# Kernel tuning notes

Measured on AMD Instinct MI355X. Metric: run time of the kernel, lower is better.

## Reference

```python
import jax, jax.numpy as jnp
import numpy as np

B, L, D = 128, 196, 512
T = 20
V, E, H, A = 10000, 256, 512, 512


def setup_inputs() -> dict:
    key = jax.random.key(0)
    ks = jax.random.split(key, 20)
    s = lambda *sh: 0.02
    inp = {
        "a": jax.random.normal(ks[0], (B, L, D), jnp.float32),
        "captions": jax.random.randint(ks[1], (B, T), 0, V),
        "lengths": jnp.full((B,), T, dtype=jnp.int64),
        "embed_W": jax.random.normal(ks[2], (V, E), jnp.float32) * 0.02,
        "Wa": jax.random.normal(ks[3], (D, A), jnp.float32) * 0.02,
        "Wh": jax.random.normal(ks[4], (H, A), jnp.float32) * 0.02,
        "Wc": jax.random.normal(ks[5], (H, A), jnp.float32) * 0.02,
        "v": jax.random.normal(ks[6], (A,), jnp.float32) * 0.02,
        "beta_W": jax.random.normal(ks[7], (H, 1), jnp.float32) * 0.02,
        "beta_b": jnp.zeros((1,), jnp.float32),
        "W_ih": jax.random.normal(ks[8], (E + D, 4 * H), jnp.float32) * 0.02,
        "W_hh": jax.random.normal(ks[9], (H, 4 * H), jnp.float32) * 0.02,
        "b_ih": jnp.zeros((4 * H,), jnp.float32),
        "b_hh": jnp.zeros((4 * H,), jnp.float32),
        "fc_W": jax.random.normal(ks[10], (H, V), jnp.float32) * 0.02,
        "fc_b": jnp.zeros((V,), jnp.float32),
        "initW_h": jax.random.normal(ks[11], (D, H), jnp.float32) * 0.02,
        "initb_h": jnp.zeros((H,), jnp.float32),
        "initW_c": jax.random.normal(ks[12], (D, H), jnp.float32) * 0.02,
        "initb_c": jnp.zeros((H,), jnp.float32),
    }
    return inp


def _decode(a, captions, embed_W, Wa, Wh, Wc, v, beta_W, beta_b,
            W_ih, W_hh, b_ih, b_hh, fc_W, fc_b,
            initW_h, initb_h, initW_c, initb_c):
    # dropout layers are treated as identity (eval mode) for a deterministic reference
    emb = embed_W[captions]                       # (B, T, E)
    mean_ctx = a.mean(axis=1)                     # (B, D)
    h0 = jnp.tanh(mean_ctx @ initW_h + initb_h)   # (B, H)
    c0 = jnp.tanh(mean_ctx @ initW_c + initb_c)
    wa = a @ Wa                                   # (B, L, A), hoisted (invariant over t)
    Hd = h0.shape[-1]

    def step(carry, x_t):
        h, c, prev_h = carry
        # dual additive attention: scores from annotations + h + prev_h (context_input)
        score = jnp.tanh(wa + (h @ Wh)[:, None, :] + (prev_h @ Wc)[:, None, :])  # (B,L,A)
        e = score @ v                                                            # (B,L)
        alpha = jax.nn.softmax(e, axis=1)
        beta = jax.nn.sigmoid(h @ beta_W + beta_b)                               # (B,1)
        ctx = beta * jnp.einsum('bl,bld->bd', alpha, a)                          # (B,D)
        # LSTMCell
        x = jnp.concatenate([x_t, ctx], axis=1)                                  # (B,E+D)
        gates = x @ W_ih + b_ih + h @ W_hh + b_hh                                # (B,4H)
        i, f, g, o = jnp.split(gates, 4, axis=1)
        c_new = jax.nn.sigmoid(f) * c + jax.nn.sigmoid(i) * jnp.tanh(g)
        h_new = jax.nn.sigmoid(o) * jnp.tanh(c_new)
        logits_t = h_new @ fc_W + fc_b                                           # (B,V)
        return (h_new, c_new, h_new), (logits_t, alpha)

    xs = jnp.swapaxes(emb[:, :T - 1, :], 0, 1)    # (T-1, B, E) time-major
    _, (logits_t, alphas_t) = jax.lax.scan(step, (h0, c0, h0), xs)
    # all lengths == T: pack_padded_sequence(batch_first=True).data is time-major flatten
    packed_logits = logits_t.reshape((T - 1) * a.shape[0], -1)                   # ((T-1)*B, V)
    alphas = jnp.swapaxes(alphas_t, 0, 1)                                        # (B, T-1, L)
    return packed_logits, alphas


def reference(a, captions, lengths, embed_W, Wa, Wh, Wc, v, beta_W, beta_b,
              W_ih, W_hh, b_ih, b_hh, fc_W, fc_b,
              initW_h, initb_h, initW_c, initb_c):
    return _decode(a, captions, embed_W, Wa, Wh, Wc, v, beta_W, beta_b,
                   W_ih, W_hh, b_ih, b_hh, fc_W, fc_b,
                   initW_h, initb_h, initW_c, initb_c)
```

## Files before the change

kernel.cpp:

```cpp
#include <hip/hip_runtime.h>
#include <hip/hip_bf16.h>
#include <math.h>

#define B_ 128
#define L_ 196
#define D_ 512
#define T_ 20
#define V_ 10000
#define E_ 256
#define H_ 512
#define A_ 512
#define TM1 19
#define ROWS (TM1*B_)
#define G4H 2048
#define KCAT 1024
#define LH 98

typedef unsigned short ushort_t;
typedef __attribute__((ext_vector_type(8))) short bf16x8;
typedef __attribute__((ext_vector_type(4))) float f32x4;

__device__ __forceinline__ float fast_tanh(float x){
    float ax = fabsf(x);
    float e = __expf(-2.f*ax);
    float r = __builtin_amdgcn_rcpf(1.f + e);
    return copysignf((1.f - e)*r, x);
}
__device__ __forceinline__ float sigmoidf_(float x){
    return __builtin_amdgcn_rcpf(1.f + __expf(-x));
}
__device__ __forceinline__ ushort_t f2b(float f){
    union{float f; unsigned u;} x; x.f = f;
    unsigned r = x.u + 0x7fffu + ((x.u>>16)&1u);
    return (ushort_t)(r>>16);
}
__device__ __forceinline__ float b2f(ushort_t h){
    union{unsigned u; float f;} x; x.u = ((unsigned)h)<<16;
    return x.f;
}
__device__ __forceinline__ float b2f_lo(unsigned u){ union{unsigned u; float f;} x; x.u = u<<16; return x.f; }
__device__ __forceinline__ float b2f_hi(unsigned u){ union{unsigned u; float f;} x; x.u = u & 0xffff0000u; return x.f; }

#define GL16(gsrc, ldst) __builtin_amdgcn_global_load_lds( \
    (const __attribute__((address_space(1))) unsigned*)(gsrc), \
    (__attribute__((address_space(3))) unsigned*)(ldst), 16, 0, 0)

__global__ __launch_bounds__(256)
void gemm_logits_k(const ushort_t* __restrict__ A, int lda,
                   const ushort_t* __restrict__ BT, int ldb,
                   float* __restrict__ C, int ldc,
                   int N, int K, const float* __restrict__ bias)
{
    __shared__ ushort_t As[2][4096];
    __shared__ ushort_t Bs[2][4096];
    int bid = blockIdx.x;
    int swz = (bid & 7)*190 + (bid >> 3);
    int mt = swz % 19, nt = swz / 19;
    if (nt >= 79) return;
    const int bm = mt*128, bn = nt*128;
    const int tid = threadIdx.x;
    const int lane = tid & 63;
    const int wave = tid >> 6;
    const int wm = (wave >> 1) * 64;
    const int wn = (wave & 1) * 64;
    const int lrow = lane & 15;
    const int lk8  = (lane >> 4) * 8;
    const int srow = tid >> 2;
    const int skq0 = (tid & 3) * 8;
    const int wbase = wave * 512;

    f32x4 acc[4][4];
    #pragma unroll
    for (int i=0;i<4;i++)
        #pragma unroll
        for (int j=0;j<4;j++) acc[i][j] = (f32x4){0.f,0.f,0.f,0.f};

    const ushort_t* Ab = A  + (size_t)(bm+srow)*lda + skq0;
    const ushort_t* Bb = BT + (size_t)(bn+srow)*ldb + skq0;

    GL16(Ab,                    &As[0][wbase]);
    GL16(Ab + (size_t)64*lda,   &As[0][2048 + wbase]);
    GL16(Bb,                    &Bs[0][wbase]);
    GL16(Bb + (size_t)64*ldb,   &Bs[0][2048 + wbase]);

    int buf = 0;
    for (int k0 = 0; k0 < K; k0 += 32) {
        asm volatile("s_waitcnt vmcnt(0)" ::: "memory");
        __syncthreads();
        if (k0 + 32 < K){
            int nb = buf ^ 1;
            GL16(Ab + k0 + 32,                  &As[nb][wbase]);
            GL16(Ab + (size_t)64*lda + k0 + 32, &As[nb][2048 + wbase]);
            GL16(Bb + k0 + 32,                  &Bs[nb][wbase]);
            GL16(Bb + (size_t)64*ldb + k0 + 32, &Bs[nb][2048 + wbase]);
        }
        bf16x8 af[4], bfr[4];
        #pragma unroll
        for (int i=0;i<4;i++) af[i]  = *(bf16x8*)&As[buf][(wm + i*16 + lrow)*32 + lk8];
        #pragma unroll
        for (int j=0;j<4;j++) bfr[j] = *(bf16x8*)&Bs[buf][(wn + j*16 + lrow)*32 + lk8];
        #pragma unroll
        for (int i=0;i<4;i++)
            #pragma unroll
            for (int j=0;j<4;j++)
                acc[i][j] = __builtin_amdgcn_mfma_f32_16x16x32_bf16(af[i], bfr[j], acc[i][j], 0, 0, 0);
        buf ^= 1;
    }

    const int rq = (lane >> 4) * 4;
    float* eps = (float*)As;
    #pragma unroll
    for (int c = 0; c < 4; ++c){
        __syncthreads();
        if ((wave >> 1) == (c >> 1)){
            const int ib = 2*(c & 1);
            #pragma unroll
            for (int ii = 0; ii < 2; ++ii){
                #pragma unroll
                for (int j = 0; j < 4; ++j){
                    #pragma unroll
                    for (int q = 0; q < 4; ++q){
                        int lr_ = ii*16 + rq + q;
                        int lc  = wn + j*16 + lrow;
                        eps[lr_*128 + lc] = acc[ib+ii][j][q];
                    }
                }
            }
        }
        __syncthreads();
        for (int it = tid; it < 1024; it += 256){
            int r = it >> 5, c4 = it & 31;
            int col0 = bn + c4*4;
            if (col0 >= N) continue;
            f32x4 vv = *(f32x4*)&eps[r*128 + c4*4];
            float* dst = &C[(size_t)(bm + 32*c + r)*ldc + col0];
            if (col0 + 3 < N){
                float4 bb = *(const float4*)(bias + col0);
                vv[0] += bb.x; vv[1] += bb.y; vv[2] += bb.z; vv[3] += bb.w;
                __builtin_nontemporal_store(vv, (f32x4*)dst);
            } else {
                for (int e=0; e<4 && col0+e < N; ++e)
                    __builtin_nontemporal_store(vv[e] + bias[col0+e], dst + e);
            }
        }
    }
}

struct GJob { const ushort_t* A; int lda; const ushort_t* BT; int ldb;
              void* C; int ldc; int N, K; const float* bias; int out_bf16; int nx; int nblk; };

__global__ __launch_bounds__(256) void gemm_dual_k(GJob j0, GJob j1){
    __shared__ ushort_t As[2][4096];
    __shared__ ushort_t Bs[2][4096];
    int bid = blockIdx.x;
    GJob jb = (bid < j0.nblk) ? j0 : j1;
    if (bid >= j0.nblk) bid -= j0.nblk;
    const int bn = (bid % jb.nx)*128, bm = (bid / jb.nx)*128;
    const int tid = threadIdx.x;
    const int lane = tid & 63;
    const int wave = tid >> 6;
    const int wm = (wave >> 1) * 64;
    const int wn = (wave & 1) * 64;
    const int lrow = lane & 15;
    const int lk8  = (lane >> 4) * 8;
    const int srow = tid >> 2;
    const int skq0 = (tid & 3) * 8;
    const int wbase = wave * 512;

    f32x4 acc[4][4];
    #pragma unroll
    for (int i=0;i<4;i++)
        #pragma unroll
        for (int j=0;j<4;j++) acc[i][j] = (f32x4){0.f,0.f,0.f,0.f};

    const ushort_t* Ab = jb.A  + (size_t)(bm+srow)*jb.lda + skq0;
    const ushort_t* Bb = jb.BT + (size_t)(bn+srow)*jb.ldb + skq0;

    GL16(Ab,                        &As[0][wbase]);
    GL16(Ab + (size_t)64*jb.lda,    &As[0][2048 + wbase]);
    GL16(Bb,                        &Bs[0][wbase]);
    GL16(Bb + (size_t)64*jb.ldb,    &Bs[0][2048 + wbase]);

    int buf = 0;
    for (int k0 = 0; k0 < jb.K; k0 += 32) {
        asm volatile("s_waitcnt vmcnt(0)" ::: "memory");
        __syncthreads();
        if (k0 + 32 < jb.K){
            int nb = buf ^ 1;
            GL16(Ab + k0 + 32,                      &As[nb][wbase]);
            GL16(Ab + (size_t)64*jb.lda + k0 + 32,  &As[nb][2048 + wbase]);
            GL16(Bb + k0 + 32,                      &Bs[nb][wbase]);
            GL16(Bb + (size_t)64*jb.ldb + k0 + 32,  &Bs[nb][2048 + wbase]);
        }
        bf16x8 af[4], bfr[4];
        #pragma unroll
        for (int i=0;i<4;i++) af[i]  = *(bf16x8*)&As[buf][(wm + i*16 + lrow)*32 + lk8];
        #pragma unroll
        for (int j=0;j<4;j++) bfr[j] = *(bf16x8*)&Bs[buf][(wn + j*16 + lrow)*32 + lk8];
        #pragma unroll
        for (int i=0;i<4;i++)
            #pragma unroll
            for (int j=0;j<4;j++)
                acc[i][j] = __builtin_amdgcn_mfma_f32_16x16x32_bf16(af[i], bfr[j], acc[i][j], 0, 0, 0);
        buf ^= 1;
    }

    const int rq = (lane >> 4) * 4;
    #pragma unroll
    for (int j=0;j<4;j++){
        int col = bn + wn + j*16 + lrow;
        if (col >= jb.N) continue;
        float bv = jb.bias ? jb.bias[col] : 0.f;
        #pragma unroll
        for (int i=0;i<4;i++){
            #pragma unroll
            for (int q=0;q<4;q++){
                int row = bm + wm + i*16 + rq + q;
                float v = acc[i][j][q] + bv;
                if (jb.out_bf16) ((ushort_t*)jb.C)[(size_t)row*jb.ldc + col] = f2b(v);
                else             ((float*)jb.C)[(size_t)row*jb.ldc + col] = v;
            }
        }
    }
}

__global__ __launch_bounds__(256) void gemm64t2(const float* __restrict__ Amcp, int lda,
                       const float* __restrict__ B0, const float* __restrict__ B1, int ldb,
                       float* __restrict__ C0, float* __restrict__ C1, int ldc,
                       const float* __restrict__ bias0, const float* __restrict__ bias1)
{
    const float* Bm  = blockIdx.z ? B1 : B0;
    float* C         = blockIdx.z ? C1 : C0;
    const float* bias= blockIdx.z ? bias1 : bias0;
    __shared__ float As[16][65];
    __shared__ float Bs[16][65];
    int bm = blockIdx.y*64, bn = blockIdx.x*64;
    int tid = threadIdx.x;
    int tx = tid & 15, ty = tid >> 4;
    const float invL = 1.f/(float)L_;
    float acc[4][4] = {};
    for (int k0 = 0; k0 < D_; k0 += 16) {
        {
            int r  = tid >> 2;
            int kq = (tid & 3) * 4;
            const float* Ap = Amcp + (size_t)(bm+r)*lda + k0 + kq;
            float4 v0 = *(const float4*)(Ap);
            float4 v1 = *(const float4*)(Ap + 65536);
            float4 v2 = *(const float4*)(Ap + 131072);
            float4 v3 = *(const float4*)(Ap + 196608);
            float4 va = make_float4((v0.x+v1.x+v2.x+v3.x)*invL, (v0.y+v1.y+v2.y+v3.y)*invL,
                                    (v0.z+v1.z+v2.z+v3.z)*invL, (v0.w+v1.w+v2.w+v3.w)*invL);
            As[kq+0][r]=va.x; As[kq+1][r]=va.y; As[kq+2][r]=va.z; As[kq+3][r]=va.w;
        }
        {
            int kk = tid >> 4;
            int nq = (tid & 15) * 4;
            float4 vb = *(const float4*)(Bm + (size_t)(k0+kk)*ldb + bn + nq);
            Bs[kk][nq+0]=vb.x; Bs[kk][nq+1]=vb.y; Bs[kk][nq+2]=vb.z; Bs[kk][nq+3]=vb.w;
        }
        __syncthreads();
        #pragma unroll
        for (int k = 0; k < 16; ++k) {
            float a0[4], b0[4];
            #pragma unroll
            for (int i=0;i<4;i++) a0[i] = As[k][ty*4+i];
            #pragma unroll
            for (int j=0;j<4;j++) b0[j] = Bs[k][tx*4+j];
            #pragma unroll
            for (int i=0;i<4;i++)
                #pragma unroll
                for (int j=0;j<4;j++)
                    acc[i][j] = fmaf(a0[i], b0[j], acc[i][j]);
        }
        __syncthreads();
    }
    #pragma unroll
    for (int i=0;i<4;i++){
        int row = bm + ty*4 + i;
        #pragma unroll
        for (int j=0;j<4;j++){
            int col = bn + tx*4 + j;
            C[(size_t)row*ldc + col] = fast_tanh(acc[i][j] + bias[col]);
        }
    }
}

struct TJob { const float* src; const float* src2; ushort_t* dst;
              int lds, Ksz, Nsz, koff, ldk, nx, nblk; };
struct PrepArgs {
    TJob j[6];
    const float* a; ushort_t* a_b; float* mcp;
    const float* b_ih; const float* b_hh; float* bias4h; unsigned* bars;
    const int* caps; const float* embW; ushort_t* xemb;
};

__global__ __launch_bounds__(256) void prep_all_k(PrepArgs P){
    __shared__ float t[32][33];
    int bid = blockIdx.x;
    const int tid = threadIdx.x;
    if (bid < 256){
        const int b = bid >> 1, half = bid & 1;
        const int quad = tid & 127;
        const int sl = tid >> 7;
        const int pi = half*2 + sl;
        const int l0 = half*LH + sl*49;
        const float* p = P.a + ((size_t)(b*L_ + l0))*D_ + quad*4;
        ushort_t* q = P.a_b + ((size_t)(b*L_ + l0))*D_ + quad*4;
        float4 s = make_float4(0.f,0.f,0.f,0.f);
        for (int l=0;l<49;l++){
            float4 v = *(const float4*)(p + (size_t)l*D_);
            s.x += v.x; s.y += v.y; s.z += v.z; s.w += v.w;
            ushort_t r[4] = {f2b(v.x),f2b(v.y),f2b(v.z),f2b(v.w)};
            *(uint2*)(q + (size_t)l*D_) = *(uint2*)r;
        }
        *(float4*)(P.mcp + (size_t)pi*65536 + (size_t)b*D_ + quad*4) = s;
        return;
    }
    bid -= 256;
    if (bid < 8128){
        int ji = 0;
        while (bid >= P.j[ji].nblk){ bid -= P.j[ji].nblk; ji++; }
        const TJob jb = P.j[ji];
        int n0 = (bid % jb.nx)*32, k0 = (bid / jb.nx)*32;
        int tx = tid & 31, ty = tid >> 5;
        #pragma unroll
        for (int kk = ty; kk < 32; kk += 8){
            int k = k0 + kk, n = n0 + tx;
            float v = 0.f;
            if (k < jb.Ksz && n < jb.Nsz){
                v = jb.src[(size_t)k*jb.lds + n];
                if (jb.src2) v += jb.src2[(size_t)k*jb.lds + n];
            }
            t[kk][tx] = v;
        }
        __syncthreads();
        #pragma unroll
        for (int nn = ty; nn < 32; nn += 8){
            int n = n0 + nn, k = k0 + tx;
            if (k < jb.Ksz) jb.dst[(size_t)n*jb.ldk + jb.koff + k] = f2b(t[tx][nn]);
        }
        return;
    }
    bid -= 8128;
    if (bid == 0){
        for (int k = tid; k < G4H; k += 256) P.bias4h[k] = P.b_ih[k] + P.b_hh[k];
        P.bars[tid] = 0u;
        return;
    }
    bid -= 1;
    int i = bid*4 + (tid >> 6);
    int lane = tid & 63;
    int tt = i / B_, b = i - tt*B_;
    int cap = P.caps[b*T_ + tt];
    float4 v = ((const float4*)(P.embW + (size_t)cap*E_))[lane];
    ushort_t r[4] = {f2b(v.x),f2b(v.y),f2b(v.z),f2b(v.w)};
    *(uint2*)(P.xemb + (size_t)i*E_ + lane*4) = *(uint2*)r;
}

__global__ __launch_bounds__(512) void hw0cvt_k(const float* __restrict__ h0f,
                        const ushort_t* __restrict__ WhcT, const float* __restrict__ beta_W,
                        ushort_t* __restrict__ xcat, float* __restrict__ hWp, float* __restrict__ bdot){
    int b = blockIdx.x, tid = threadIdx.x;
    int lane = tid & 63, wave = tid >> 6;
    __shared__ ushort_t hls[512];
    __shared__ float rr[8];
    float hv = h0f[b*H_ + tid];
    ushort_t hb = f2b(hv);
    xcat[(size_t)b*KCAT + D_ + tid] = hb;
    hls[tid] = hb;
    hWp[(size_t)(b*2+1)*512 + tid] = 0.f;
    float dv = hv * beta_W[tid];
    #pragma unroll
    for (int off=32; off; off>>=1) dv += __shfl_down(dv, off);
    if (lane==0) rr[wave] = dv;
    __syncthreads();
    if (tid == 0){
        float s = rr[0]+rr[1]+rr[2]+rr[3]+rr[4]+rr[5]+rr[6]+rr[7];
        bdot[b*2] = s; bdot[b*2+1] = 0.f;
    }
    int wn = wave * 64;
    int col16 = lane & 15;
    int khi = (lane >> 4) * 8;
    bool a_on = (col16 == 0);
    f32x4 acc[4];
    #pragma unroll
    for (int f=0;f<4;f++) acc[f] = (f32x4){0.f,0.f,0.f,0.f};
    for (int kk=0; kk<16; kk++){
        bf16x8 af = (bf16x8){0,0,0,0,0,0,0,0};
        if (a_on) af = *(const bf16x8*)&hls[kk*32 + khi];
        #pragma unroll
        for (int f=0;f<4;f++){
            bf16x8 bf = *(const bf16x8*)(WhcT + (size_t)(wn + f*16 + col16)*512 + kk*32 + khi);
            acc[f] = __builtin_amdgcn_mfma_f32_16x16x32_bf16(af, bf, acc[f], 0, 0, 0);
        }
    }
    if (lane < 16){
        #pragma unroll
        for (int f=0;f<4;f++) hWp[(size_t)(b*2+0)*512 + wn + f*16 + lane] = acc[f][0];
    }
}

__global__ __launch_bounds__(1024) void mega2_k(const ushort_t* __restrict__ wa,
                        const ushort_t* __restrict__ a_b,
                        const float* __restrict__ v,
                        const float* __restrict__ beta_W, const float* __restrict__ beta_b,
                        const ushort_t* __restrict__ WhcT,
                        const float* __restrict__ gp, const float* __restrict__ embWih,
                        float* __restrict__ cbuf, float* __restrict__ hWp,
                        ushort_t* __restrict__ xcat, ushort_t* __restrict__ Hall,
                        float* __restrict__ alphas_out, float* __restrict__ ebuf,
                        unsigned* __restrict__ ebar, float* __restrict__ bdot, int t)
{
    const int b = blockIdx.x, half = blockIdx.y;
    const int tid = threadIdx.x;
    const int lane = tid & 63, wave = tid >> 6;
    __shared__ ushort_t hls[256];
    __shared__ float red[32];
    __shared__ float al_s[224];
    __shared__ float4 part4[16][64];

    if (t > 0){
        float dv = 0.f;
        if (tid < 256){
            const int j = half*256 + tid;
            const float* eb = embWih + ((size_t)((t-1)*B_ + b))*G4H;
            float gi = eb[j], gf = eb[H_+j], gg = eb[2*H_+j], go = eb[3*H_+j];
            #pragma unroll
            for (int ks=0; ks<8; ks++){
                const float* g = gp + ((size_t)(ks*B_ + b))*G4H;
                gi += g[j]; gf += g[H_+j]; gg += g[2*H_+j]; go += g[3*H_+j];
            }
            float ig = sigmoidf_(gi), fg = sigmoidf_(gf);
            float g2 = fast_tanh(gg), og = sigmoidf_(go);
            float c = fg*cbuf[b*H_+j] + ig*g2;
            float h = og*fast_tanh(c);
            cbuf[b*H_+j] = c;
            ushort_t hb = f2b(h);
            xcat[(size_t)b*KCAT + D_ + j] = hb;
            Hall[((size_t)(t-1)*B_ + b)*H_ + j] = hb;
            hls[tid] = hb;
            dv = h * beta_W[j];
        }
        #pragma unroll
        for (int off=32; off; off>>=1) dv += __shfl_down(dv, off);
        if (lane==0) red[wave] = dv;
        __syncthreads();
        int wn = wave * 32;
        int col16 = lane & 15;
        int khi = (lane >> 4) * 8;
        bool a_on = (col16 == 0);
        f32x4 acc[2];
        acc[0] = (f32x4){0.f,0.f,0.f,0.f};
        acc[1] = (f32x4){0.f,0.f,0.f,0.f};
        #pragma unroll
        for (int kk=0; kk<8; kk++){
            bf16x8 af = (bf16x8){0,0,0,0,0,0,0,0};
            if (a_on) af = *(const bf16x8*)&hls[kk*32 + khi];
            #pragma unroll
            for (int f=0;f<2;f++){
                bf16x8 bf = *(const bf16x8*)(WhcT + (size_t)(wn + f*16 + col16)*512 + half*256 + kk*32 + khi);
                acc[f] = __builtin_amdgcn_mfma_f32_16x16x32_bf16(af, bf, acc[f], 0, 0, 0);
            }
        }
        if (lane < 16){
            #pragma unroll
            for (int f=0;f<2;f++) hWp[(size_t)(b*2+half)*512 + wn + f*16 + lane] = acc[f][0];
        }
    }
    __syncthreads();
    if (tid == 0){
        if (t > 0){
            float s = 0.f;
            #pragma unroll
            for (int w=0; w<16; w++) s += red[w];
            bdot[b*2+half] = s;
        }
        __threadfence();
        atomicAdd(&ebar[b], 1u);
        const unsigned tgt = 2u*(unsigned)(2*t+1);
        while (__hip_atomic_load(&ebar[b], __ATOMIC_ACQUIRE, __HIP_MEMORY_SCOPE_AGENT) < tgt)
            __builtin_amdgcn_s_sleep(1);
    }
    __syncthreads();
    {
        const float* hp0 = hWp + (size_t)(b*2+0)*512 + lane*8;
        const float* hp1 = hWp + (size_t)(b*2+1)*512 + lane*8;
        float4 p00 = *(const float4*)hp0, p01 = *(const float4*)(hp0+4);
        float4 p10 = *(const float4*)hp1, p11 = *(const float4*)(hp1+4);
        float4 hw0 = make_float4(p00.x+p10.x, p00.y+p10.y, p00.z+p10.z, p00.w+p10.w);
        float4 hw1 = make_float4(p01.x+p11.x, p01.y+p11.y, p01.z+p11.z, p01.w+p11.w);
        const float* vp = v + lane*8;
        float4 v0 = *(const float4*)vp, v1 = *(const float4*)(vp+4);
        const int l0 = half*LH;
        for (int r = wave; r < LH; r += 16){
            int4 raw = *(const int4*)(wa + (((size_t)(b*L_ + l0 + r))<<9) + lane*8);
            const unsigned* u = (const unsigned*)&raw;
            float s;
            s  = fast_tanh(b2f_lo(u[0]) + hw0.x)*v0.x;
            s += fast_tanh(b2f_hi(u[0]) + hw0.y)*v0.y;
            s += fast_tanh(b2f_lo(u[1]) + hw0.z)*v0.z;
            s += fast_tanh(b2f_hi(u[1]) + hw0.w)*v0.w;
            s += fast_tanh(b2f_lo(u[2]) + hw1.x)*v1.x;
            s += fast_tanh(b2f_hi(u[2]) + hw1.y)*v1.y;
            s += fast_tanh(b2f_lo(u[3]) + hw1.z)*v1.z;
            s += fast_tanh(b2f_hi(u[3]) + hw1.w)*v1.w;
            #pragma unroll
            for (int off=32; off; off>>=1) s += __shfl_down(s, off);
            if (lane==0) ebuf[b*L_ + l0 + r] = s;
        }
    }
    __syncthreads();
    if (tid == 0){
        __threadfence();
        atomicAdd(&ebar[b], 1u);
        const unsigned tgt = 2u*(unsigned)(2*t+2);
        while (__hip_atomic_load(&ebar[b], __ATOMIC_ACQUIRE, __HIP_MEMORY_SCOPE_AGENT) < tgt)
            __builtin_amdgcn_s_sleep(1);
    }
    __syncthreads();
    float ev = (tid < L_) ? ebuf[b*L_ + tid] : -3.0e38f;
    float wmax = ev;
    #pragma unroll
    for (int off=32; off; off>>=1) wmax = fmaxf(wmax, __shfl_down(wmax, off));
    if (lane==0) red[wave] = wmax;
    __syncthreads();
    float m = red[0];
    #pragma unroll
    for (int w=1; w<16; w++) m = fmaxf(m, red[w]);
    float pr = (tid < L_) ? __expf(ev - m) : 0.f;
    float wsum = pr;
    #pragma unroll
    for (int off=32; off; off>>=1) wsum += __shfl_down(wsum, off);
    if (lane==0) red[16+wave] = wsum;
    __syncthreads();
    float sum = red[16];
    #pragma unroll
    for (int w=1; w<16; w++) sum += red[16+w];
    float inv = 1.f / sum;
    if (tid < L_) al_s[tid] = pr*inv;
    const int l0 = half*LH;
    if (tid >= l0 && tid < l0 + LH)
        __builtin_nontemporal_store(pr*inv, alphas_out + (size_t)b*TM1*L_ + (size_t)t*L_ + tid);
    __syncthreads();
    {
        const int dg = tid & 63;
        const int lr = tid >> 6;
        const int d0 = half*256 + dg*4;
        const ushort_t* pa = a_b + (((size_t)(b*L_))<<9) + d0;
        float4 s = make_float4(0.f,0.f,0.f,0.f);
        for (int l = lr; l < L_; l += 16){
            uint2 av = *(const uint2*)(pa + ((size_t)l<<9));
            float al = al_s[l];
            s.x = fmaf(al, b2f_lo(av.x), s.x);
            s.y = fmaf(al, b2f_hi(av.x), s.y);
            s.z = fmaf(al, b2f_lo(av.y), s.z);
            s.w = fmaf(al, b2f_hi(av.y), s.w);
        }
        part4[lr][dg] = s;
        __syncthreads();
        if (tid < 64){
            float beta = sigmoidf_(bdot[b*2] + bdot[b*2+1] + beta_b[0]);
            float4 r = make_float4(0.f,0.f,0.f,0.f);
            #pragma unroll
            for (int q=0;q<16;q++){
                float4 pv = part4[q][tid];
                r.x += pv.x; r.y += pv.y; r.z += pv.z; r.w += pv.w;
            }
            unsigned lo = (unsigned)f2b(beta*r.x) | (((unsigned)f2b(beta*r.y))<<16);
            unsigned hi = (unsigned)f2b(beta*r.z) | (((unsigned)f2b(beta*r.w))<<16);
            uint2 pk; pk.x = lo; pk.y = hi;
            *(uint2*)(xcat + (size_t)b*KCAT + half*256 + tid*4) = pk;
        }
    }
}

__global__ __launch_bounds__(256) void gates_k(const ushort_t* __restrict__ xcat,
                        const ushort_t* __restrict__ WcatT, float* __restrict__ gp){
    __shared__ ushort_t As[128*32];
    __shared__ ushort_t Bs[64*32];
    const int bn = blockIdx.x*64;
    const int ks = blockIdx.y;
    const int tid = threadIdx.x;
    const int lane = tid & 63, wave = tid >> 6;
    const int wm = wave*32;
    const int lrow = lane & 15;
    const int lk8 = (lane >> 4) * 8;
    f32x4 acc[2][4];
    #pragma unroll
    for (int i=0;i<2;i++)
        #pragma unroll
        for (int j=0;j<4;j++) acc[i][j] = (f32x4){0.f,0.f,0.f,0.f};

    for (int kk = 0; kk < 4; ++kk){
        int k0 = ks*128 + kk*32;
        int c0 = 2*tid;
        int r0 = c0 >> 2,  kq0 = (c0 & 3)*8;
        int r1 = (c0+1) >> 2, kq1 = ((c0+1) & 3)*8;
        int4 a0 = *(const int4*)(xcat + (size_t)r0*KCAT + k0 + kq0);
        int4 a1 = *(const int4*)(xcat + (size_t)r1*KCAT + k0 + kq1);
        int rb = tid >> 2, kqb = (tid & 3)*8;
        int4 b0 = *(const int4*)(WcatT + (size_t)(bn+rb)*KCAT + k0 + kqb);
        __syncthreads();
        *(int4*)&As[r0*32 + kq0] = a0;
        *(int4*)&As[r1*32 + kq1] = a1;
        *(int4*)&Bs[rb*32 + kqb] = b0;
        __syncthreads();
        bf16x8 af[2], bfr[4];
        #pragma unroll
        for (int i=0;i<2;i++) af[i] = *(bf16x8*)&As[(wm + i*16 + lrow)*32 + lk8];
        #pragma unroll
        for (int j=0;j<4;j++) bfr[j] = *(bf16x8*)&Bs[(j*16 + lrow)*32 + lk8];
        #pragma unroll
        for (int i=0;i<2;i++)
            #pragma unroll
            for (int j=0;j<4;j++)
                acc[i][j] = __builtin_amdgcn_mfma_f32_16x16x32_bf16(af[i], bfr[j], acc[i][j], 0, 0, 0);
    }
    const int rq = (lane >> 4) * 4;
    #pragma unroll
    for (int i=0;i<2;i++){
        #pragma unroll
        for (int j=0;j<4;j++){
            int gcol = bn + j*16 + lrow;
            #pragma unroll
            for (int q=0;q<4;q++){
                int grow = wm + i*16 + rq + q;
                gp[((size_t)(ks*B_ + grow))*G4H + gcol] = acc[i][j][q];
            }
        }
    }
}

__global__ __launch_bounds__(512) void lstmfin_k(const float* __restrict__ gp, const float* __restrict__ embWih,
                       const float* __restrict__ cbuf, ushort_t* __restrict__ Hall){
    int b = blockIdx.x, j = threadIdx.x;
    const float* eb = embWih + ((size_t)(18*B_ + b))*G4H;
    float gi = eb[j], gf = eb[H_+j], gg = eb[2*H_+j], go = eb[3*H_+j];
    #pragma unroll
    for (int ks=0; ks<8; ks++){
        const float* g = gp + ((size_t)(ks*B_ + b))*G4H;
        gi += g[j]; gf += g[H_+j]; gg += g[2*H_+j]; go += g[3*H_+j];
    }
    float ig = sigmoidf_(gi), fg = sigmoidf_(gf);
    float g2 = fast_tanh(gg), og = sigmoidf_(go);
    float c = fg*cbuf[b*H_+j] + ig*g2;
    float h = og*fast_tanh(c);
    Hall[((size_t)18*B_ + b)*H_ + j] = f2b(h);
}

extern "C" void kernel_launch(void* const* d_in, const int* in_sizes, int n_in,
                              void* d_out, int out_size, void* d_ws, size_t ws_size,
                              hipStream_t stream) {
    const float* a      = (const float*)d_in[0];
    const int*   caps   = (const int*)  d_in[1];
    const float* embW   = (const float*)d_in[3];
    const float* Wa     = (const float*)d_in[4];
    const float* Wh     = (const float*)d_in[5];
    const float* Wc     = (const float*)d_in[6];
    const float* v      = (const float*)d_in[7];
    const float* beta_W = (const float*)d_in[8];
    const float* beta_b = (const float*)d_in[9];
    const float* W_ih   = (const float*)d_in[10];
    const float* W_hh   = (const float*)d_in[11];
    const float* b_ih   = (const float*)d_in[12];
    const float* b_hh   = (const float*)d_in[13];
    const float* fc_W   = (const float*)d_in[14];
    const float* fc_b   = (const float*)d_in[15];
    const float* iWh    = (const float*)d_in[16];
    const float* ibh    = (const float*)d_in[17];
    const float* iWc    = (const float*)d_in[18];
    const float* ibc    = (const float*)d_in[19];

    float* out    = (float*)d_out;
    float* alphas = out + (size_t)ROWS*V_;

    char* ob = (char*)d_out;
    ushort_t* wa_b   = (ushort_t*)(ob);
    ushort_t* a_b    = (ushort_t*)(ob + 25690112);
    float*    embWih = (float*)   (ob + 51380224);

    char* wb = (char*)d_ws;
    float* mcp      = (float*)(wb);
    float* bdot     = (float*)(wb + 1048576);
    float* cbuf     = (float*)(wb + 1052672);
    float* h0f      = (float*)(wb + 1314816);
    float* hWp      = (float*)(wb + 1576960);
    float* ebuf     = (float*)(wb + 2101248);
    float* bias4h   = (float*)(wb + 2203648);
    unsigned* bars  = (unsigned*)(wb + 2211840);
    float* gp       = (float*)(wb + 2215936);
    ushort_t* xcat_b = (ushort_t*)(wb + 10604544);
    ushort_t* xemb_b = (ushort_t*)(wb + 10866688);
    ushort_t* Hall   = (ushort_t*)(wb + 12111872);
    ushort_t* WaT    = (ushort_t*)(wb + 14602240);
    ushort_t* WhcT   = (ushort_t*)(wb + 15126528);
    ushort_t* WihT   = (ushort_t*)(wb + 15650816);
    ushort_t* WcatT  = (ushort_t*)(wb + 16699392);
    ushort_t* fcWT   = (ushort_t*)(wb + 20893696);

    PrepArgs P;
    P.j[0] = { Wa,   nullptr, WaT,  512, 512, 512,  0,   512,  16, 256 };
    P.j[1] = { Wh,   Wc,      WhcT, 512, 512, 512,  0,   512,  16, 256 };
    P.j[2] = { W_ih, nullptr, WihT, G4H, 256, G4H,  0,   256,  64, 512 };
    P.j[3] = { W_ih + (size_t)E_*G4H, nullptr, WcatT, G4H, 512, G4H, 0,   KCAT, 64, 1024 };
    P.j[4] = { W_hh, nullptr, WcatT, G4H, 512, G4H,  512, KCAT, 64, 1024 };
    P.j[5] = { fc_W, nullptr, fcWT, V_,  512, V_,   0,   512,  316, 5056 };
    P.a = a; P.a_b = a_b; P.mcp = mcp;
    P.b_ih = b_ih; P.b_hh = b_hh; P.bias4h = bias4h; P.bars = bars;
    P.caps = caps; P.embW = embW; P.xemb = xemb_b;
    prep_all_k<<<8993, 256, 0, stream>>>(P);

    gemm64t2<<<dim3(8,2,2), 256, 0, stream>>>(mcp, D_, iWh, iWc, H_, h0f, cbuf, H_, ibh, ibc);
    hw0cvt_k<<<B_, 512, 0, stream>>>(h0f, WhcT, beta_W, xcat_b, hWp, bdot);

    GJob g0 = { a_b,    512, WaT,  512, wa_b,   512, 512,  512, nullptr, 1, 4,  784 };
    GJob g1 = { xemb_b, 256, WihT, 256, embWih, G4H, G4H,  256, bias4h,  0, 16, 304 };
    gemm_dual_k<<<1088, 256, 0, stream>>>(g0, g1);

    for (int t = 0; t < TM1; ++t){
        mega2_k<<<dim3(B_,2), 1024, 0, stream>>>(wa_b, a_b, v, beta_W, beta_b, WhcT,
                                                 gp, embWih, cbuf, hWp, xcat_b, Hall,
                                                 alphas, ebuf, bars, bdot, t);
        gates_k<<<dim3(32,8), 256, 0, stream>>>(xcat_b, WcatT, gp);
    }
    lstmfin_k<<<B_, 512, 0, stream>>>(gp, embWih, cbuf, Hall);

    gemm_logits_k<<<dim3(1520), 256, 0, stream>>>(Hall, H_, fcWT, H_, out, V_, V_, H_, fc_b);
}
```

Measured before the change: 977.4 us.

## Compute full LSTM update redundantly per half-block to drop one cross-block barrier

Both half-blocks of each batch row now compute the full LSTM cell update and the full h·[Wh|Wc] projection, keeping the result in shared memory. This removes the first global spin barrier per timestep, which existed only to exchange partial projections and beta dot products between the halves. The cell state is double-buffered by timestep parity so the two halves cannot race on it, and each block reuses its own attention scores from shared memory instead of re-reading them from global memory. The cost is duplicated gate reads and MFMA work in each block.

```diff
diff --git a/kernel.cpp b/kernel.cpp
--- a/kernel.cpp
+++ b/kernel.cpp
@@ -359,7 +359,7 @@
 
 __global__ __launch_bounds__(512) void hw0cvt_k(const float* __restrict__ h0f,
                         const ushort_t* __restrict__ WhcT, const float* __restrict__ beta_W,
-                        ushort_t* __restrict__ xcat, float* __restrict__ hWp, float* __restrict__ bdot){
+                        ushort_t* __restrict__ xcat, float* __restrict__ hW0, float* __restrict__ bdot0){
     int b = blockIdx.x, tid = threadIdx.x;
     int lane = tid & 63, wave = tid >> 6;
     __shared__ ushort_t hls[512];
@@ -368,16 +368,13 @@
     ushort_t hb = f2b(hv);
     xcat[(size_t)b*KCAT + D_ + tid] = hb;
     hls[tid] = hb;
-    hWp[(size_t)(b*2+1)*512 + tid] = 0.f;
     float dv = hv * beta_W[tid];
     #pragma unroll
     for (int off=32; off; off>>=1) dv += __shfl_down(dv, off);
     if (lane==0) rr[wave] = dv;
     __syncthreads();
-    if (tid == 0){
-        float s = rr[0]+rr[1]+rr[2]+rr[3]+rr[4]+rr[5]+rr[6]+rr[7];
-        bdot[b*2] = s; bdot[b*2+1] = 0.f;
-    }
+    if (tid == 0)
+        bdot0[b] = rr[0]+rr[1]+rr[2]+rr[3]+rr[4]+rr[5]+rr[6]+rr[7];
     int wn = wave * 64;
     int col16 = lane & 15;
     int khi = (lane >> 4) * 8;
@@ -396,7 +393,7 @@
     }
     if (lane < 16){
         #pragma unroll
-        for (int f=0;f<4;f++) hWp[(size_t)(b*2+0)*512 + wn + f*16 + lane] = acc[f][0];
+        for (int f=0;f<4;f++) hW0[(size_t)b*512 + wn + f*16 + lane] = acc[f][0];
     }
 }
 
@@ -406,23 +403,27 @@
                         const float* __restrict__ beta_W, const float* __restrict__ beta_b,
                         const ushort_t* __restrict__ WhcT,
                         const float* __restrict__ gp, const float* __restrict__ embWih,
-                        float* __restrict__ cbuf, float* __restrict__ hWp,
+                        float* __restrict__ cbuf2, const float* __restrict__ hW0,
+                        const float* __restrict__ bdot0,
                         ushort_t* __restrict__ xcat, ushort_t* __restrict__ Hall,
                         float* __restrict__ alphas_out, float* __restrict__ ebuf,
-                        unsigned* __restrict__ ebar, float* __restrict__ bdot, int t)
+                        unsigned* __restrict__ ebar, int t)
 {
     const int b = blockIdx.x, half = blockIdx.y;
     const int tid = threadIdx.x;
     const int lane = tid & 63, wave = tid >> 6;
-    __shared__ ushort_t hls[256];
+    __shared__ ushort_t hls[512];
+    __shared__ float hWl[512];
     __shared__ float red[32];
     __shared__ float al_s[224];
+    __shared__ float e_s[LH];
+    __shared__ float bdot_s;
     __shared__ float4 part4[16][64];
 
     if (t > 0){
         float dv = 0.f;
-        if (tid < 256){
-            const int j = half*256 + tid;
+        if (tid < 512){
+            const int j = tid;
             const float* eb = embWih + ((size_t)((t-1)*B_ + b))*G4H;
             float gi = eb[j], gf = eb[H_+j], gg = eb[2*H_+j], go = eb[3*H_+j];
             #pragma unroll
@@ -432,19 +433,27 @@
             }
             float ig = sigmoidf_(gi), fg = sigmoidf_(gf);
             float g2 = fast_tanh(gg), og = sigmoidf_(go);
-            float c = fg*cbuf[b*H_+j] + ig*g2;
+            float c = fg*cbuf2[((t-1)&1)*65536 + b*H_+j] + ig*g2;
             float h = og*fast_tanh(c);
-            cbuf[b*H_+j] = c;
             ushort_t hb = f2b(h);
-            xcat[(size_t)b*KCAT + D_ + j] = hb;
-            Hall[((size_t)(t-1)*B_ + b)*H_ + j] = hb;
-            hls[tid] = hb;
+            if (half == 0){
+                cbuf2[(t&1)*65536 + b*H_+j] = c;
+                xcat[(size_t)b*KCAT + D_ + j] = hb;
+                Hall[((size_t)(t-1)*B_ + b)*H_ + j] = hb;
+            }
+            hls[j] = hb;
             dv = h * beta_W[j];
         }
         #pragma unroll
         for (int off=32; off; off>>=1) dv += __shfl_down(dv, off);
         if (lane==0) red[wave] = dv;
         __syncthreads();
+        if (tid == 0){
+            float s = 0.f;
+            #pragma unroll
+            for (int w=0; w<8; w++) s += red[w];
+            bdot_s = s;
+        }
         int wn = wave * 32;
         int col16 = lane & 15;
         int khi = (lane >> 4) * 8;
@@ -453,42 +462,27 @@
         acc[0] = (f32x4){0.f,0.f,0.f,0.f};
         acc[1] = (f32x4){0.f,0.f,0.f,0.f};
         #pragma unroll
-        for (int kk=0; kk<8; kk++){
+        for (int kk=0; kk<16; kk++){
             bf16x8 af = (bf16x8){0,0,0,0,0,0,0,0};
             if (a_on) af = *(const bf16x8*)&hls[kk*32 + khi];
             #pragma unroll
             for (int f=0;f<2;f++){
-                bf16x8 bf = *(const bf16x8*)(WhcT + (size_t)(wn + f*16 + col16)*512 + half*256 + kk*32 + khi);
+                bf16x8 bf = *(const bf16x8*)(WhcT + (size_t)(wn + f*16 + col16)*512 + kk*32 + khi);
                 acc[f] = __builtin_amdgcn_mfma_f32_16x16x32_bf16(af, bf, acc[f], 0, 0, 0);
             }
         }
         if (lane < 16){
             #pragma unroll
-            for (int f=0;f<2;f++) hWp[(size_t)(b*2+half)*512 + wn + f*16 + lane] = acc[f][0];
-        }
-    }
-    __syncthreads();
-    if (tid == 0){
-        if (t > 0){
-            float s = 0.f;
-            #pragma unroll
-            for (int w=0; w<16; w++) s += red[w];
-            bdot[b*2+half] = s;
-        }
-        __threadfence();
-        atomicAdd(&ebar[b], 1u);
-        const unsigned tgt = 2u*(unsigned)(2*t+1);
-        while (__hip_atomic_load(&ebar[b], __ATOMIC_ACQUIRE, __HIP_MEMORY_SCOPE_AGENT) < tgt)
-            __builtin_amdgcn_s_sleep(1);
+            for (int f=0;f<2;f++) hWl[wn + f*16 + lane] = acc[f][0];
+        }
+    } else {
+        if (tid < 512) hWl[tid] = hW0[(size_t)b*512 + tid];
+        if (tid == 0) bdot_s = bdot0[b];
     }
     __syncthreads();
     {
-        const float* hp0 = hWp + (size_t)(b*2+0)*512 + lane*8;
-        const float* hp1 = hWp + (size_t)(b*2+1)*512 + lane*8;
-        float4 p00 = *(const float4*)hp0, p01 = *(const float4*)(hp0+4);
-        float4 p10 = *(const float4*)hp1, p11 = *(const float4*)(hp1+4);
-        float4 hw0 = make_float4(p00.x+p10.x, p00.y+p10.y, p00.z+p10.z, p00.w+p10.w);
-        float4 hw1 = make_float4(p01.x+p11.x, p01.y+p11.y, p01.z+p11.z, p01.w+p11.w);
+        float4 hw0v = *(float4*)&hWl[lane*8];
+        float4 hw1v = *(float4*)&hWl[lane*8 + 4];
         const float* vp = v + lane*8;
         float4 v0 = *(const float4*)vp, v1 = *(const float4*)(vp+4);
         const int l0 = half*LH;
@@ -496,29 +490,34 @@
             int4 raw = *(const int4*)(wa + (((size_t)(b*L_ + l0 + r))<<9) + lane*8);
             const unsigned* u = (const unsigned*)&raw;
             float s;
-            s  = fast_tanh(b2f_lo(u[0]) + hw0.x)*v0.x;
-            s += fast_tanh(b2f_hi(u[0]) + hw0.y)*v0.y;
-            s += fast_tanh(b2f_lo(u[1]) + hw0.z)*v0.z;
-            s += fast_tanh(b2f_hi(u[1]) + hw0.w)*v0.w;
-            s += fast_tanh(b2f_lo(u[2]) + hw1.x)*v1.x;
-            s += fast_tanh(b2f_hi(u[2]) + hw1.y)*v1.y;
-            s += fast_tanh(b2f_lo(u[3]) + hw1.z)*v1.z;
-            s += fast_tanh(b2f_hi(u[3]) + hw1.w)*v1.w;
+            s  = fast_tanh(b2f_lo(u[0]) + hw0v.x)*v0.x;
+            s += fast_tanh(b2f_hi(u[0]) + hw0v.y)*v0.y;
+            s += fast_tanh(b2f_lo(u[1]) + hw0v.z)*v0.z;
+            s += fast_tanh(b2f_hi(u[1]) + hw0v.w)*v0.w;
+            s += fast_tanh(b2f_lo(u[2]) + hw1v.x)*v1.x;
+            s += fast_tanh(b2f_hi(u[2]) + hw1v.y)*v1.y;
+            s += fast_tanh(b2f_lo(u[3]) + hw1v.z)*v1.z;
+            s += fast_tanh(b2f_hi(u[3]) + hw1v.w)*v1.w;
             #pragma unroll
             for (int off=32; off; off>>=1) s += __shfl_down(s, off);
-            if (lane==0) ebuf[b*L_ + l0 + r] = s;
+            if (lane==0){ ebuf[b*L_ + l0 + r] = s; e_s[r] = s; }
         }
     }
     __syncthreads();
     if (tid == 0){
         __threadfence();
         atomicAdd(&ebar[b], 1u);
-        const unsigned tgt = 2u*(unsigned)(2*t+2);
+        const unsigned tgt = 2u*(unsigned)(t+1);
         while (__hip_atomic_load(&ebar[b], __ATOMIC_ACQUIRE, __HIP_MEMORY_SCOPE_AGENT) < tgt)
             __builtin_amdgcn_s_sleep(1);
     }
     __syncthreads();
-    float ev = (tid < L_) ? ebuf[b*L_ + tid] : -3.0e38f;
+    const int l0 = half*LH;
+    float ev = -3.0e38f;
+    if (tid < L_){
+        int loc = tid - l0;
+        ev = (loc >= 0 && loc < LH) ? e_s[loc] : ebuf[b*L_ + tid];
+    }
     float wmax = ev;
     #pragma unroll
     for (int off=32; off; off>>=1) wmax = fmaxf(wmax, __shfl_down(wmax, off));
@@ -538,7 +537,6 @@
     for (int w=1; w<16; w++) sum += red[16+w];
     float inv = 1.f / sum;
     if (tid < L_) al_s[tid] = pr*inv;
-    const int l0 = half*LH;
     if (tid >= l0 && tid < l0 + LH)
         __builtin_nontemporal_store(pr*inv, alphas_out + (size_t)b*TM1*L_ + (size_t)t*L_ + tid);
     __syncthreads();
@@ -559,7 +557,7 @@
         part4[lr][dg] = s;
         __syncthreads();
         if (tid < 64){
-            float beta = sigmoidf_(bdot[b*2] + bdot[b*2+1] + beta_b[0]);
+            float beta = sigmoidf_(bdot_s + beta_b[0]);
             float4 r = make_float4(0.f,0.f,0.f,0.f);
             #pragma unroll
             for (int q=0;q<16;q++){
@@ -632,7 +630,7 @@
 }
 
 __global__ __launch_bounds__(512) void lstmfin_k(const float* __restrict__ gp, const float* __restrict__ embWih,
-                       const float* __restrict__ cbuf, ushort_t* __restrict__ Hall){
+                       const float* __restrict__ cbuf2, ushort_t* __restrict__ Hall){
     int b = blockIdx.x, j = threadIdx.x;
     const float* eb = embWih + ((size_t)(18*B_ + b))*G4H;
     float gi = eb[j], gf = eb[H_+j], gg = eb[2*H_+j], go = eb[3*H_+j];
@@ -643,7 +641,7 @@
     }
     float ig = sigmoidf_(gi), fg = sigmoidf_(gf);
     float g2 = fast_tanh(gg), og = sigmoidf_(go);
-    float c = fg*cbuf[b*H_+j] + ig*g2;
+    float c = fg*cbuf2[b*H_+j] + ig*g2;
     float h = og*fast_tanh(c);
     Hall[((size_t)18*B_ + b)*H_ + j] = f2b(h);
 }
@@ -681,10 +679,10 @@
 
     char* wb = (char*)d_ws;
     float* mcp      = (float*)(wb);
-    float* bdot     = (float*)(wb + 1048576);
-    float* cbuf     = (float*)(wb + 1052672);
-    float* h0f      = (float*)(wb + 1314816);
-    float* hWp      = (float*)(wb + 1576960);
+    float* bdot0    = (float*)(wb + 1048576);
+    float* cbuf2    = (float*)(wb + 1052672);
+    float* h0f      = (float*)(wb + 1576960);
+    float* hW0      = (float*)(wb + 1839104);
     float* ebuf     = (float*)(wb + 2101248);
     float* bias4h   = (float*)(wb + 2203648);
     unsigned* bars  = (unsigned*)(wb + 2211840);
@@ -710,8 +708,8 @@
     P.caps = caps; P.embW = embW; P.xemb = xemb_b;
     prep_all_k<<<8993, 256, 0, stream>>>(P);
 
-    gemm64t2<<<dim3(8,2,2), 256, 0, stream>>>(mcp, D_, iWh, iWc, H_, h0f, cbuf, H_, ibh, ibc);
-    hw0cvt_k<<<B_, 512, 0, stream>>>(h0f, WhcT, beta_W, xcat_b, hWp, bdot);
+    gemm64t2<<<dim3(8,2,2), 256, 0, stream>>>(mcp, D_, iWh, iWc, H_, h0f, cbuf2, H_, ibh, ibc);
+    hw0cvt_k<<<B_, 512, 0, stream>>>(h0f, WhcT, beta_W, xcat_b, hW0, bdot0);
 
     GJob g0 = { a_b,    512, WaT,  512, wa_b,   512, 512,  512, nullptr, 1, 4,  784 };
     GJob g1 = { xemb_b, 256, WihT, 256, embWih, G4H, G4H,  256, bias4h,  0, 16, 304 };
@@ -719,11 +717,11 @@
 
     for (int t = 0; t < TM1; ++t){
         mega2_k<<<dim3(B_,2), 1024, 0, stream>>>(wa_b, a_b, v, beta_W, beta_b, WhcT,
-                                                 gp, embWih, cbuf, hWp, xcat_b, Hall,
-                                                 alphas, ebuf, bars, bdot, t);
+                                                 gp, embWih, cbuf2, hW0, bdot0, xcat_b, Hall,
+                                                 alphas, ebuf, bars, t);
         gates_k<<<dim3(32,8), 256, 0, stream>>>(xcat_b, WcatT, gp);
     }
-    lstmfin_k<<<B_, 512, 0, stream>>>(gp, embWih, cbuf, Hall);
+    lstmfin_k<<<B_, 512, 0, stream>>>(gp, embWih, cbuf2, Hall);
 
     gemm_logits_k<<<dim3(1520), 256, 0, stream>>>(Hall, H_, fcWT, H_, out, V_, V_, H_, fc_b);
 }
```

After: 966.9 us. Within noise of the previous version (-1.1%).
